# Performance work log

Hardware: AMD Instinct MI355X
Metric: run time of the kernel (lower is better)

Reference implementation:

```python
import jax, jax.numpy as jnp
import numpy as np

H = 2048        # hidden_size
NH = 32         # num_attention_heads
HD = H // NH    # head_dim
I = 8192        # intermediate_size
L = 2           # num_hidden_layers
B, S = 1, 2048
EPS = 1e-5


def _layernorm(x, gamma):
    # keras LayerNormalization(center=False): mean-subtract, var-normalize, scale by gamma (no beta)
    mu = jnp.mean(x, axis=-1, keepdims=True)
    var = jnp.mean(jnp.square(x - mu), axis=-1, keepdims=True)
    return (x - mu) * jax.lax.rsqrt(var + EPS) * gamma


def _gelu_tanh(x):
    return 0.5 * x * (1.0 + jnp.tanh(0.7978845608028654 * x * (1.0 + 0.044715 * x * x)))


def setup_inputs() -> dict:
    key = jax.random.key(0)
    ks = jax.random.split(key, 12)
    sd = 0.02
    inputs_embeds = jax.random.normal(ks[0], (B, S, H), dtype=jnp.float32)
    attention_mask = jnp.tril(jnp.ones((S, S), dtype=bool))[None, None]  # causal [1,1,S,S]
    return {
        "inputs_embeds": inputs_embeds,
        "attention_mask": attention_mask,
        "Wq": jax.random.normal(ks[1], (L, H, H), jnp.float32) * sd,
        "Wk": jax.random.normal(ks[2], (L, H, H), jnp.float32) * sd,
        "Wv": jax.random.normal(ks[3], (L, H, H), jnp.float32) * sd,
        "Wo": jax.random.normal(ks[4], (L, H, H), jnp.float32) * sd,
        "bo": jnp.zeros((L, H), jnp.float32),
        "W1": jax.random.normal(ks[5], (L, H, I), jnp.float32) * sd,
        "W2": jax.random.normal(ks[6], (L, I, H), jnp.float32) * sd,
        "b2": jnp.zeros((L, H), jnp.float32),
        "g1": jnp.ones((L, H), jnp.float32),
        "g2": jnp.ones((L, H), jnp.float32),
        "gf": jnp.ones((H,), jnp.float32),
    }


def _forward(inputs_embeds, attention_mask, Wq, Wk, Wv, Wo, bo, W1, W2, b2, g1, g2, gf):
    x = inputs_embeds
    scale = 1.0 / jnp.sqrt(jnp.float32(HD))
    for l in range(L):
        # --- attention block ---
        h = _layernorm(x, g1[l])
        q = h @ Wq[l]
        k = h @ Wk[l]
        v = h @ Wv[l]
        # split heads: [B,S,H] -> [B,NH,S,HD]
        q = q.reshape(B, S, NH, HD).transpose(0, 2, 1, 3)
        k = k.reshape(B, S, NH, HD).transpose(0, 2, 1, 3)
        v = v.reshape(B, S, NH, HD).transpose(0, 2, 1, 3)
        scores = jnp.einsum("bhqd,bhkd->bhqk", q, k) * scale
        scores = jnp.where(attention_mask, scores, jnp.float32(-1e9))
        probs = jax.nn.softmax(scores, axis=-1)
        ctx = jnp.einsum("bhqk,bhkd->bhqd", probs, v)
        ctx = ctx.transpose(0, 2, 1, 3).reshape(B, S, H)
        x = x + (ctx @ Wo[l] + bo[l])
        # --- MLP block ---
        h = _layernorm(x, g2[l])
        h = _gelu_tanh(h @ W1[l]) @ W2[l] + b2[l]
        x = x + h
    return _layernorm(x, gf)


def reference(inputs_embeds, attention_mask, Wq, Wk, Wv, Wo, bo, W1, W2, b2, g1, g2, gf):
    return _forward(inputs_embeds, attention_mask, Wq, Wk, Wv, Wo, bo, W1, W2, b2, g1, g2, gf)
```

## Files before the change

kernel.cpp:

```cpp
#include <hip/hip_runtime.h>
#include <hip/hip_bf16.h>
#include <stdint.h>


#define H_   2048
#define NH_  32
#define HD_  64
#define I_   8192
#define L_   2
#define S_   2048
#define EPS_ 1e-5f

typedef _Float16 f16;
typedef __attribute__((ext_vector_type(8))) _Float16 f16x8;
typedef __attribute__((ext_vector_type(4))) float   f32x4;

#define BF16_PROBE 0x3F803F80u

static __device__ __forceinline__ float bf2f(unsigned short b) {
  return __uint_as_float(((unsigned int)b) << 16);
}

static __device__ __forceinline__ float gelu_f(float x) {
  float y = 0.7978845608028654f * x * (1.0f + 0.044715f * x * x);
  return x / (1.0f + __expf(-2.0f * y));
}

#define GLDS(gp, lp)                                                          \
  __builtin_amdgcn_global_load_lds(                                           \
      (const __attribute__((address_space(1))) unsigned int*)(gp),            \
      (__attribute__((address_space(3))) unsigned int*)(lp), 16, 0, 0)

__global__ __launch_bounds__(256) void embed2f_k(const void* __restrict__ e,
                                                 float* __restrict__ xf,
                                                 const unsigned int* __restrict__ probe) {
  bool isbf = (*probe == BF16_PROBE);
  int i = (blockIdx.x * 256 + threadIdx.x) * 4;
  float4 o;
  if (isbf) {
    uint2 d = *(const uint2*)((const unsigned short*)e + i);
    o.x = bf2f((unsigned short)(d.x & 0xffff));
    o.y = bf2f((unsigned short)(d.x >> 16));
    o.z = bf2f((unsigned short)(d.y & 0xffff));
    o.w = bf2f((unsigned short)(d.y >> 16));
  } else {
    o = *(const float4*)((const float*)e + i);
  }
  *(float4*)(xf + i) = o;
}

template <int OUT_FINAL>
__global__ __launch_bounds__(256) void ln_k(const float* __restrict__ x,
                                            const void* __restrict__ gammav,
                                            size_t geoff,
                                            void* __restrict__ outv,
                                            const unsigned int* __restrict__ probe) {
  bool isbf = (*probe == BF16_PROBE);
  int row = blockIdx.x, t = threadIdx.x;
  const float* xr = x + (size_t)row * H_;
  float4 a = ((const float4*)xr)[t];
  float4 b = ((const float4*)xr)[t + 256];
  float s  = a.x + a.y + a.z + a.w + b.x + b.y + b.z + b.w;
  float ss = a.x*a.x + a.y*a.y + a.z*a.z + a.w*a.w
           + b.x*b.x + b.y*b.y + b.z*b.z + b.w*b.w;
#pragma unroll
  for (int m = 32; m >= 1; m >>= 1) { s += __shfl_xor(s, m); ss += __shfl_xor(ss, m); }
  __shared__ float red[8];
  if ((t & 63) == 0) { red[t >> 6] = s; red[4 + (t >> 6)] = ss; }
  __syncthreads();
  s  = red[0] + red[1] + red[2] + red[3];
  ss = red[4] + red[5] + red[6] + red[7];
  float mu   = s * (1.0f / H_);
  float rstd = rsqrtf(ss * (1.0f / H_) - mu * mu + EPS_);
  float va[8] = {a.x, a.y, a.z, a.w, b.x, b.y, b.z, b.w};
#pragma unroll
  for (int hh = 0; hh < 2; ++hh) {
    int cbase = (hh == 0) ? t * 4 : (t + 256) * 4;
#pragma unroll
    for (int j = 0; j < 4; ++j) {
      int c = cbase + j;
      float g = isbf ? bf2f(((const unsigned short*)gammav)[geoff + c])
                     : ((const float*)gammav)[geoff + c];
      float o = (va[hh * 4 + j] - mu) * rstd * g;
      size_t idx = (size_t)row * H_ + c;
      if (OUT_FINAL) {
        if (isbf) ((__hip_bfloat16*)outv)[idx] = __float2bfloat16(o);
        else      ((float*)outv)[idx] = o;
      } else {
        ((f16*)outv)[idx] = (f16)o;
      }
    }
  }
}

__global__ __launch_bounds__(256) void transp_k(const void* __restrict__ in,
                                                size_t eoff,
                                                f16* __restrict__ out, int R, int C,
                                                const unsigned int* __restrict__ probe) {
  bool isbf = (*probe == BF16_PROBE);
  __shared__ __attribute__((aligned(16))) f16 tile[64][72];
  int t = threadIdx.x;
  int r0 = blockIdx.y * 64, c0 = blockIdx.x * 64;
#pragma unroll
  for (int it = 0; it < 2; ++it) {
    int idx = it * 256 + t;
    int r = idx >> 3, c8 = (idx & 7) * 8;
    size_t goff = eoff + (size_t)(r0 + r) * C + c0 + c8;
    if (isbf) {
      uint4 d = *(const uint4*)((const unsigned short*)in + goff);
      unsigned int dw[4] = {d.x, d.y, d.z, d.w};
#pragma unroll
      for (int p = 0; p < 4; ++p) {
        tile[r][c8 + 2 * p]     = (f16)bf2f((unsigned short)(dw[p] & 0xffff));
        tile[r][c8 + 2 * p + 1] = (f16)bf2f((unsigned short)(dw[p] >> 16));
      }
    } else {
      float4 fa = *(const float4*)((const float*)in + goff);
      float4 fb = *(const float4*)((const float*)in + goff + 4);
      tile[r][c8 + 0] = (f16)fa.x; tile[r][c8 + 1] = (f16)fa.y;
      tile[r][c8 + 2] = (f16)fa.z; tile[r][c8 + 3] = (f16)fa.w;
      tile[r][c8 + 4] = (f16)fb.x; tile[r][c8 + 5] = (f16)fb.y;
      tile[r][c8 + 6] = (f16)fb.z; tile[r][c8 + 7] = (f16)fb.w;
    }
  }
  __syncthreads();
#pragma unroll
  for (int it = 0; it < 2; ++it) {
    int idx = it * 256 + t;
    int rn = idx >> 3, k8 = (idx & 7) * 8;
    f16x8 o;
#pragma unroll
    for (int j = 0; j < 8; ++j) o[j] = tile[k8 + j][rn];
    *(f16x8*)(out + (size_t)(c0 + rn) * R + r0 + k8) = o;
  }
}

template <int MODE>
__global__ __launch_bounds__(256) void gemm_k(const f16* __restrict__ A,
                                              const f16* __restrict__ Bt,
                                              f16* __restrict__ Cf,
                                              float* __restrict__ xres,
                                              const void* __restrict__ biasv,
                                              size_t beoff,
                                              int N, int K,
                                              const unsigned int* __restrict__ probe) {
  __shared__ __attribute__((aligned(16))) f16 As[128 * 32];
  __shared__ __attribute__((aligned(16))) f16 Bs[128 * 32];
  int t = threadIdx.x;
  int lane = t & 63, w = t >> 6;
  int col = lane & 15, quad = lane >> 4;
  int tm = blockIdx.x * 128, tn = blockIdx.y * 128;
  int wm = (w & 1) * 64, wn = (w >> 1) * 64;

  f32x4 acc[4][4];
#pragma unroll
  for (int i = 0; i < 4; ++i)
#pragma unroll
    for (int j = 0; j < 4; ++j) acc[i][j] = (f32x4){0.f, 0.f, 0.f, 0.f};

  const f16* Ab = A  + (size_t)(tm + (t >> 2)) * K + (t & 3) * 8;
  const f16* Bb = Bt + (size_t)(tn + (t >> 2)) * K + (t & 3) * 8;
  f16* Al = As + t * 8;
  f16* Bl = Bs + t * 8;

  for (int k0 = 0; k0 < K; k0 += 32) {
    GLDS(Ab + k0, Al);
    GLDS(Ab + (size_t)64 * K + k0, Al + 2048);
    GLDS(Bb + k0, Bl);
    GLDS(Bb + (size_t)64 * K + k0, Bl + 2048);
    __syncthreads();
    f16x8 af[4], bf[4];
#pragma unroll
    for (int i = 0; i < 4; ++i)
      af[i] = *(const f16x8*)(As + (wm + i * 16 + col) * 32 + quad * 8);
#pragma unroll
    for (int j = 0; j < 4; ++j)
      bf[j] = *(const f16x8*)(Bs + (wn + j * 16 + col) * 32 + quad * 8);
#pragma unroll
    for (int i = 0; i < 4; ++i)
#pragma unroll
      for (int j = 0; j < 4; ++j)
        acc[i][j] = __builtin_amdgcn_mfma_f32_16x16x32_f16(af[i], bf[j], acc[i][j], 0, 0, 0);
    __syncthreads();
  }

  bool isbf = false;
  if (MODE == 2) isbf = (*probe == BF16_PROBE);
#pragma unroll
  for (int i = 0; i < 4; ++i) {
    int row = tm + wm + i * 16 + quad * 4;
#pragma unroll
    for (int j = 0; j < 4; ++j) {
      int cg = tn + wn + j * 16 + col;
#pragma unroll
      for (int r = 0; r < 4; ++r) {
        float v = acc[i][j][r];
        if (MODE == 1) v = gelu_f(v);
        if (MODE <= 1) {
          Cf[(size_t)(row + r) * N + cg] = (f16)v;
        } else {
          float bb = isbf ? bf2f(((const unsigned short*)biasv)[beoff + cg])
                          : ((const float*)biasv)[beoff + cg];
          size_t idx = (size_t)(row + r) * N + cg;
          xres[idx] += v + bb;
        }
      }
    }
  }
}

__global__ __launch_bounds__(256) void attn_k(const f16* __restrict__ qkv,
                                              f16* __restrict__ ctx) {
  __shared__ __attribute__((aligned(16))) f16 Ks[64 * 72];
  __shared__ __attribute__((aligned(16))) f16 Vt[64 * 72];
  __shared__ __attribute__((aligned(16))) f16 Ps[4 * 16 * 72];
  const int RS = 3 * H_;
  int t = threadIdx.x, w = t >> 6, lane = t & 63;
  int col = lane & 15, quad = lane >> 4;
  int head = blockIdx.y;
  int qt = (gridDim.x - 1) - blockIdx.x;
  int q0 = qt * 64;

  int qrow = q0 + w * 16 + col;
  const f16* qp = qkv + (size_t)qrow * RS + head * HD_ + quad * 8;
  f16x8 qf0 = *(const f16x8*)qp;
  f16x8 qf1 = *(const f16x8*)(qp + 32);

  f32x4 O[4];
#pragma unroll
  for (int ht = 0; ht < 4; ++ht) O[ht] = (f32x4){0.f, 0.f, 0.f, 0.f};
  f32x4 mrow = (f32x4){-1e30f, -1e30f, -1e30f, -1e30f};
  f32x4 lrow = (f32x4){0.f, 0.f, 0.f, 0.f};
  f16* pw = Ps + w * 16 * 72;

  for (int c = 0; c <= qt; ++c) {
    int k0 = c * 64;
#pragma unroll
    for (int it = 0; it < 2; ++it) {
      int idx = it * 256 + t;
      int r = idx >> 3, c8 = (idx & 7) * 8;
      const f16* kp = qkv + (size_t)(k0 + r) * RS + H_ + head * HD_ + c8;
      *(f16x8*)(Ks + r * 72 + c8) = *(const f16x8*)kp;
      const f16* vp = qkv + (size_t)(k0 + r) * RS + 2 * H_ + head * HD_ + c8;
      f16x8 vv = *(const f16x8*)vp;
#pragma unroll
      for (int j = 0; j < 8; ++j) Vt[(c8 + j) * 72 + r] = vv[j];
    }
    __syncthreads();

    f32x4 s[4];
#pragma unroll
    for (int nt = 0; nt < 4; ++nt) {
      const f16* kb = Ks + (nt * 16 + col) * 72 + quad * 8;
      f16x8 b0 = *(const f16x8*)kb;
      f16x8 b1 = *(const f16x8*)(kb + 32);
      f32x4 z = (f32x4){0.f, 0.f, 0.f, 0.f};
      z = __builtin_amdgcn_mfma_f32_16x16x32_f16(qf0, b0, z, 0, 0, 0);
      z = __builtin_amdgcn_mfma_f32_16x16x32_f16(qf1, b1, z, 0, 0, 0);
      s[nt] = z;
    }
    int rq = q0 + w * 16 + quad * 4;
#pragma unroll
    for (int nt = 0; nt < 4; ++nt)
#pragma unroll
      for (int r = 0; r < 4; ++r) {
        float sv = s[nt][r] * 0.125f;
        if (k0 + nt * 16 + col > rq + r) sv = -1e30f;
        s[nt][r] = sv;
      }
    f32x4 mx;
#pragma unroll
    for (int r = 0; r < 4; ++r)
      mx[r] = fmaxf(fmaxf(s[0][r], s[1][r]), fmaxf(s[2][r], s[3][r]));
#pragma unroll
    for (int m = 1; m <= 8; m <<= 1)
#pragma unroll
      for (int r = 0; r < 4; ++r) mx[r] = fmaxf(mx[r], __shfl_xor(mx[r], m));
    f32x4 mnew, alpha, rs;
#pragma unroll
    for (int r = 0; r < 4; ++r) {
      mnew[r]  = fmaxf(mrow[r], mx[r]);
      alpha[r] = __expf(mrow[r] - mnew[r]);
      rs[r] = 0.f;
    }
#pragma unroll
    for (int nt = 0; nt < 4; ++nt)
#pragma unroll
      for (int r = 0; r < 4; ++r) {
        float p = __expf(s[nt][r] - mnew[r]);
        s[nt][r] = p;
        rs[r] += p;
      }
#pragma unroll
    for (int m = 1; m <= 8; m <<= 1)
#pragma unroll
      for (int r = 0; r < 4; ++r) rs[r] += __shfl_xor(rs[r], m);
#pragma unroll
    for (int r = 0; r < 4; ++r) {
      lrow[r] = lrow[r] * alpha[r] + rs[r];
      mrow[r] = mnew[r];
    }
#pragma unroll
    for (int ht = 0; ht < 4; ++ht)
#pragma unroll
      for (int r = 0; r < 4; ++r) O[ht][r] *= alpha[r];

#pragma unroll
    for (int nt = 0; nt < 4; ++nt)
#pragma unroll
      for (int r = 0; r < 4; ++r)
        pw[(quad * 4 + r) * 72 + nt * 16 + col] = (f16)s[nt][r];
    const f16* pr = pw + col * 72 + quad * 8;
    f16x8 p0 = *(const f16x8*)pr;
    f16x8 p1 = *(const f16x8*)(pr + 32);
#pragma unroll
    for (int ht = 0; ht < 4; ++ht) {
      const f16* vb = Vt + (ht * 16 + col) * 72 + quad * 8;
      f16x8 v0 = *(const f16x8*)vb;
      f16x8 v1 = *(const f16x8*)(vb + 32);
      O[ht] = __builtin_amdgcn_mfma_f32_16x16x32_f16(p0, v0, O[ht], 0, 0, 0);
      O[ht] = __builtin_amdgcn_mfma_f32_16x16x32_f16(p1, v1, O[ht], 0, 0, 0);
    }
    __syncthreads();
  }

#pragma unroll
  for (int ht = 0; ht < 4; ++ht)
#pragma unroll
    for (int r = 0; r < 4; ++r) {
      int row = q0 + w * 16 + quad * 4 + r;
      int cg = head * HD_ + ht * 16 + col;
      ctx[(size_t)row * H_ + cg] = (f16)(O[ht][r] / lrow[r]);
    }
}

extern "C" void kernel_launch(void* const* d_in, const int* in_sizes, int n_in,
                              void* d_out, int out_size, void* d_ws, size_t ws_size,
                              hipStream_t stream) {
  const void* embeds = d_in[0];
  const void* Wq = d_in[2];
  const void* Wk = d_in[3];
  const void* Wv = d_in[4];
  const void* Wo = d_in[5];
  const void* bo = d_in[6];
  const void* W1 = d_in[7];
  const void* W2 = d_in[8];
  const void* b2 = d_in[9];
  const void* g1 = d_in[10];
  const void* g2 = d_in[11];
  const void* gf = d_in[12];
  const unsigned int* probe = (const unsigned int*)g1;

  char* W = (char*)d_ws;
  float* xf  = (float*)(W);
  f16* hbuf  = (f16*)(W + (16ull << 20));
  f16* qkvb  = (f16*)(W + (24ull << 20));
  f16* ctxb  = (f16*)(W + (48ull << 20));
  f16* m1b   = (f16*)(W + (24ull << 20));
  f16* Wt    = (f16*)(W + (56ull << 20));
  (void)in_sizes; (void)n_in; (void)out_size; (void)ws_size;

  embed2f_k<<<S_ * H_ / 1024, 256, 0, stream>>>(embeds, xf, probe);

  for (int l = 0; l < L_; ++l) {
    size_t wo = (size_t)l * H_ * H_;
    ln_k<0><<<S_, 256, 0, stream>>>(xf, g1, (size_t)l * H_, hbuf, probe);
    transp_k<<<dim3(H_ / 64, H_ / 64), 256, 0, stream>>>(Wq, wo, Wt, H_, H_, probe);
    transp_k<<<dim3(H_ / 64, H_ / 64), 256, 0, stream>>>(Wk, wo, Wt + (size_t)H_ * H_, H_, H_, probe);
    transp_k<<<dim3(H_ / 64, H_ / 64), 256, 0, stream>>>(Wv, wo, Wt + 2ull * H_ * H_, H_, H_, probe);
    gemm_k<0><<<dim3(S_ / 128, 3 * H_ / 128), 256, 0, stream>>>(hbuf, Wt, qkvb, nullptr, nullptr, 0, 3 * H_, H_, probe);
    attn_k<<<dim3(S_ / 64, NH_), 256, 0, stream>>>(qkvb, ctxb);
    transp_k<<<dim3(H_ / 64, H_ / 64), 256, 0, stream>>>(Wo, wo, Wt, H_, H_, probe);
    gemm_k<2><<<dim3(S_ / 128, H_ / 128), 256, 0, stream>>>(ctxb, Wt, nullptr, xf, bo, (size_t)l * H_, H_, H_, probe);
    ln_k<0><<<S_, 256, 0, stream>>>(xf, g2, (size_t)l * H_, hbuf, probe);
    transp_k<<<dim3(I_ / 64, H_ / 64), 256, 0, stream>>>(W1, (size_t)l * H_ * I_, Wt, H_, I_, probe);
    gemm_k<1><<<dim3(S_ / 128, I_ / 128), 256, 0, stream>>>(hbuf, Wt, m1b, nullptr, nullptr, 0, I_, H_, probe);
    transp_k<<<dim3(H_ / 64, I_ / 64), 256, 0, stream>>>(W2, (size_t)l * I_ * H_, Wt, I_, H_, probe);
    gemm_k<2><<<dim3(S_ / 128, H_ / 128), 256, 0, stream>>>(m1b, Wt, nullptr, xf, b2, (size_t)l * H_, H_, I_, probe);
  }
  ln_k<1><<<S_, 256, 0, stream>>>(xf, gf, 0, d_out, probe);
}
```

Before: 1.630 ms.

## Split-K the residual GEMMs with atomic accumulation and batch QKV weight transposes

The Wo and W2 projection GEMMs (N=2048) only launched 256 blocks, so each is now split 4 ways along K using blockIdx.z, with partial results added to the fp32 residual via atomicAdd and the bias applied only by the z=0 slice. The three Q/K/V weight transposes are merged into one launch with a z dimension. This targets low occupancy on the narrow GEMMs and launch overhead, at the cost of atomic traffic on the residual buffer and nondeterministic fp32 summation order.

```diff
diff --git a/kernel.cpp b/kernel.cpp
--- a/kernel.cpp
+++ b/kernel.cpp
@@ -93,11 +93,20 @@
   }
 }
 
-__global__ __launch_bounds__(256) void transp_k(const void* __restrict__ in,
+template <int NSRC>
+__global__ __launch_bounds__(256) void transp_k(const void* __restrict__ p0,
+                                                const void* __restrict__ p1,
+                                                const void* __restrict__ p2,
                                                 size_t eoff,
                                                 f16* __restrict__ out, int R, int C,
                                                 const unsigned int* __restrict__ probe) {
   bool isbf = (*probe == BF16_PROBE);
+  const void* in = p0;
+  if (NSRC == 3) {
+    if (blockIdx.z == 1) in = p1;
+    if (blockIdx.z == 2) in = p2;
+    out += (size_t)blockIdx.z * R * C;
+  }
   __shared__ __attribute__((aligned(16))) f16 tile[64][72];
   int t = threadIdx.x;
   int r0 = blockIdx.y * 64, c0 = blockIdx.x * 64;
@@ -142,7 +151,7 @@
                                               float* __restrict__ xres,
                                               const void* __restrict__ biasv,
                                               size_t beoff,
-                                              int N, int K,
+                                              int N, int K, int ldk,
                                               const unsigned int* __restrict__ probe) {
   __shared__ __attribute__((aligned(16))) f16 As[128 * 32];
   __shared__ __attribute__((aligned(16))) f16 Bs[128 * 32];
@@ -151,6 +160,7 @@
   int col = lane & 15, quad = lane >> 4;
   int tm = blockIdx.x * 128, tn = blockIdx.y * 128;
   int wm = (w & 1) * 64, wn = (w >> 1) * 64;
+  int kbase = blockIdx.z * K;
 
   f32x4 acc[4][4];
 #pragma unroll
@@ -158,16 +168,16 @@
 #pragma unroll
     for (int j = 0; j < 4; ++j) acc[i][j] = (f32x4){0.f, 0.f, 0.f, 0.f};
 
-  const f16* Ab = A  + (size_t)(tm + (t >> 2)) * K + (t & 3) * 8;
-  const f16* Bb = Bt + (size_t)(tn + (t >> 2)) * K + (t & 3) * 8;
+  const f16* Ab = A  + (size_t)(tm + (t >> 2)) * ldk + kbase + (t & 3) * 8;
+  const f16* Bb = Bt + (size_t)(tn + (t >> 2)) * ldk + kbase + (t & 3) * 8;
   f16* Al = As + t * 8;
   f16* Bl = Bs + t * 8;
 
   for (int k0 = 0; k0 < K; k0 += 32) {
     GLDS(Ab + k0, Al);
-    GLDS(Ab + (size_t)64 * K + k0, Al + 2048);
+    GLDS(Ab + (size_t)64 * ldk + k0, Al + 2048);
     GLDS(Bb + k0, Bl);
-    GLDS(Bb + (size_t)64 * K + k0, Bl + 2048);
+    GLDS(Bb + (size_t)64 * ldk + k0, Bl + 2048);
     __syncthreads();
     f16x8 af[4], bf[4];
 #pragma unroll
@@ -201,8 +211,9 @@
         } else {
           float bb = isbf ? bf2f(((const unsigned short*)biasv)[beoff + cg])
                           : ((const float*)biasv)[beoff + cg];
+          if (blockIdx.z != 0) bb = 0.f;
           size_t idx = (size_t)(row + r) * N + cg;
-          xres[idx] += v + bb;
+          atomicAdd(&xres[idx], v + bb);
         }
       }
     }
@@ -365,18 +376,16 @@
   for (int l = 0; l < L_; ++l) {
     size_t wo = (size_t)l * H_ * H_;
     ln_k<0><<<S_, 256, 0, stream>>>(xf, g1, (size_t)l * H_, hbuf, probe);
-    transp_k<<<dim3(H_ / 64, H_ / 64), 256, 0, stream>>>(Wq, wo, Wt, H_, H_, probe);
-    transp_k<<<dim3(H_ / 64, H_ / 64), 256, 0, stream>>>(Wk, wo, Wt + (size_t)H_ * H_, H_, H_, probe);
-    transp_k<<<dim3(H_ / 64, H_ / 64), 256, 0, stream>>>(Wv, wo, Wt + 2ull * H_ * H_, H_, H_, probe);
-    gemm_k<0><<<dim3(S_ / 128, 3 * H_ / 128), 256, 0, stream>>>(hbuf, Wt, qkvb, nullptr, nullptr, 0, 3 * H_, H_, probe);
+    transp_k<3><<<dim3(H_ / 64, H_ / 64, 3), 256, 0, stream>>>(Wq, Wk, Wv, wo, Wt, H_, H_, probe);
+    gemm_k<0><<<dim3(S_ / 128, 3 * H_ / 128), 256, 0, stream>>>(hbuf, Wt, qkvb, nullptr, nullptr, 0, 3 * H_, H_, H_, probe);
     attn_k<<<dim3(S_ / 64, NH_), 256, 0, stream>>>(qkvb, ctxb);
-    transp_k<<<dim3(H_ / 64, H_ / 64), 256, 0, stream>>>(Wo, wo, Wt, H_, H_, probe);
-    gemm_k<2><<<dim3(S_ / 128, H_ / 128), 256, 0, stream>>>(ctxb, Wt, nullptr, xf, bo, (size_t)l * H_, H_, H_, probe);
+    transp_k<1><<<dim3(H_ / 64, H_ / 64), 256, 0, stream>>>(Wo, nullptr, nullptr, wo, Wt, H_, H_, probe);
+    gemm_k<2><<<dim3(S_ / 128, H_ / 128, 4), 256, 0, stream>>>(ctxb, Wt, nullptr, xf, bo, (size_t)l * H_, H_, H_ / 4, H_, probe);
     ln_k<0><<<S_, 256, 0, stream>>>(xf, g2, (size_t)l * H_, hbuf, probe);
-    transp_k<<<dim3(I_ / 64, H_ / 64), 256, 0, stream>>>(W1, (size_t)l * H_ * I_, Wt, H_, I_, probe);
-    gemm_k<1><<<dim3(S_ / 128, I_ / 128), 256, 0, stream>>>(hbuf, Wt, m1b, nullptr, nullptr, 0, I_, H_, probe);
-    transp_k<<<dim3(H_ / 64, I_ / 64), 256, 0, stream>>>(W2, (size_t)l * I_ * H_, Wt, I_, H_, probe);
-    gemm_k<2><<<dim3(S_ / 128, H_ / 128), 256, 0, stream>>>(m1b, Wt, nullptr, xf, b2, (size_t)l * H_, H_, I_, probe);
+    transp_k<1><<<dim3(I_ / 64, H_ / 64), 256, 0, stream>>>(W1, nullptr, nullptr, (size_t)l * H_ * I_, Wt, H_, I_, probe);
+    gemm_k<1><<<dim3(S_ / 128, I_ / 128), 256, 0, stream>>>(hbuf, Wt, m1b, nullptr, nullptr, 0, I_, H_, H_, probe);
+    transp_k<1><<<dim3(H_ / 64, I_ / 64), 256, 0, stream>>>(W2, nullptr, nullptr, (size_t)l * I_ * H_, Wt, I_, H_, probe);
+    gemm_k<2><<<dim3(S_ / 128, H_ / 128, 4), 256, 0, stream>>>(m1b, Wt, nullptr, xf, b2, (size_t)l * H_, H_, I_ / 4, I_, probe);
   }
   ln_k<1><<<S_, 256, 0, stream>>>(xf, gf, 0, d_out, probe);
 }
```

After: 1.672 ms. +2.5%, slower.
